# Kernel tuning notes

Hardware: AMD Instinct MI355X
Metric: run time of the kernel (lower is better)

The kernel has to match this reference:

```python
import jax, jax.numpy as jnp
import numpy as np

EMB = 256
HEADS = 8

def setup_inputs() -> dict:
    key = jax.random.key(0)
    k1, k2, k3, k4, k5 = jax.random.split(key, 5)
    b, t = 8, 1024
    scale = 1.0 / np.sqrt(EMB)
    x = jax.random.normal(k1, (b, t, EMB), dtype=jnp.float32)
    # nn.Linear weights stored as [out, in]; we store [in, out] for x @ W
    Wk = jax.random.normal(k2, (EMB, EMB * HEADS), dtype=jnp.float32) * scale
    Wq = jax.random.normal(k3, (EMB, EMB * HEADS), dtype=jnp.float32) * scale
    Wv = jax.random.normal(k4, (EMB, EMB * HEADS), dtype=jnp.float32) * scale
    Wu = jax.random.normal(k5, (EMB * HEADS, EMB), dtype=jnp.float32) * scale
    return {"x": x, "Wq": Wq, "Wk": Wk, "Wv": Wv, "Wu": Wu}

def reference(x, Wq, Wk, Wv, Wu):
    b, t, e = x.shape
    h, d = HEADS, EMB  # per-head dim equals emb_in in this module
    q = (x @ Wq).reshape(b, t, h, d)
    k = (x @ Wk).reshape(b, t, h, d)
    v = (x @ Wv).reshape(b, t, h, d)
    inv4 = d ** (-0.25)
    q = q * inv4
    k = k * inv4
    # scores: [b, h, t, t]
    dot = jnp.einsum('bthd,bshd->bhts', q, k)
    attn = jax.nn.softmax(dot, axis=-1)
    out = jnp.einsum('bhts,bshd->bthd', attn, v).reshape(b, t, h * d)
    return out @ Wu
```

## Files before the change

kernel.cpp:

```cpp
#include <hip/hip_runtime.h>
#include <stdint.h>

typedef unsigned short u16;
typedef __bf16 bf16x8 __attribute__((ext_vector_type(8)));
typedef float f32x4 __attribute__((ext_vector_type(4)));
typedef u16 u16x8 __attribute__((ext_vector_type(8)));

#define MFMA16(a, b, c) __builtin_amdgcn_mfma_f32_16x16x32_bf16((a), (b), (c), 0, 0, 0)

__device__ __forceinline__ u16 f2bf(float f) {
  union { float f; uint32_t u; } v; v.f = f;
  uint32_t u = v.u;
  return (u16)((u + 0x7FFFu + ((u >> 16) & 1u)) >> 16);
}

__device__ __forceinline__ uint32_t pk2(float a, float b) {
  union { __bf16 h[2]; uint32_t u; } v;
  v.h[0] = (__bf16)a; v.h[1] = (__bf16)b;
  return v.u;
}

__device__ __forceinline__ void gload_lds16(const u16* g, u16* l) {
  __builtin_amdgcn_global_load_lds((const __attribute__((address_space(1))) void*)g,
                                   (__attribute__((address_space(3))) void*)l, 16, 0, 0);
}

__global__ __launch_bounds__(256) void prep(const float* __restrict__ x,
                                            const float* __restrict__ Wq,
                                            const float* __restrict__ Wk,
                                            const float* __restrict__ Wv,
                                            const float* __restrict__ Wu,
                                            u16* __restrict__ xb,
                                            u16* __restrict__ WtQ,
                                            u16* __restrict__ WtK,
                                            u16* __restrict__ WtV,
                                            u16* __restrict__ Wut) {
  const int bid = blockIdx.x;
  if (bid < 2048) {
    int i = bid * 256 + threadIdx.x;
    float4 v = ((const float4*)x)[i];
    ushort4 o;
    o.x = f2bf(v.x); o.y = f2bf(v.y); o.z = f2bf(v.z); o.w = f2bf(v.w);
    ((ushort4*)xb)[i] = o;
    return;
  }
  __shared__ float t32[32][33];
  const float* in;
  u16* out;
  int R, C, idx;
  float scale;
  if (bid < 2560)      { idx = bid - 2048; in = Wq; out = WtQ; R = 256;  C = 2048; scale = 0.25f; }
  else if (bid < 3072) { idx = bid - 2560; in = Wk; out = WtK; R = 256;  C = 2048; scale = 0.25f; }
  else if (bid < 3584) { idx = bid - 3072; in = Wv; out = WtV; R = 256;  C = 2048; scale = 1.0f; }
  else                 { idx = bid - 3584; in = Wu; out = Wut; R = 2048; C = 256;  scale = 1.0f; }
  int bx, by;
  if (bid < 3584) { bx = idx & 63; by = idx >> 6; }
  else            { bx = idx & 7;  by = idx >> 3; }
  const int c0 = bx * 32, r0 = by * 32;
  const int tx = threadIdx.x & 31, ty = threadIdx.x >> 5;
  #pragma unroll
  for (int i = 0; i < 32; i += 8)
    t32[ty + i][tx] = in[(size_t)(r0 + ty + i) * C + c0 + tx] * scale;
  __syncthreads();
  #pragma unroll
  for (int i = 0; i < 32; i += 8)
    out[(size_t)(c0 + ty + i) * R + r0 + tx] = f2bf(t32[tx][ty + i]);
}

__global__ __launch_bounds__(256, 2) void gemm_qkv(const u16* __restrict__ A,
                                                   const u16* __restrict__ Bt,
                                                   u16* __restrict__ Qm,
                                                   u16* __restrict__ Km,
                                                   u16* __restrict__ Vtm) {
  __shared__ __attribute__((aligned(16))) u16 As[128 * 32];
  __shared__ __attribute__((aligned(16))) u16 Bs[128 * 32];
  const int tid = threadIdx.x;
  const int lane = tid & 63;
  const int w = tid >> 6;
  const int wr = w >> 1, wc = w & 1;
  const int row0 = blockIdx.y * 128, col0 = blockIdx.x * 128;
  const int rr = lane & 15, kg = lane >> 4;

  f32x4 acc[4][4];
  const f32x4 fz = {0.f, 0.f, 0.f, 0.f};
  #pragma unroll
  for (int m = 0; m < 4; ++m)
    #pragma unroll
    for (int n = 0; n < 4; ++n) acc[m][n] = fz;

  for (int k0 = 0; k0 < 256; k0 += 32) {
    #pragma unroll
    for (int c = 0; c < 2; ++c) {
      int Lb = c * 256 + w * 64;
      int L = Lb + lane;
      int r = L >> 2, cc = L & 3;
      gload_lds16(&A[(size_t)(row0 + r) * 256 + k0 + cc * 8], &As[Lb << 3]);
      gload_lds16(&Bt[(size_t)(col0 + r) * 256 + k0 + cc * 8], &Bs[Lb << 3]);
    }
    __syncthreads();
    bf16x8 af[4], bfr[4];
    #pragma unroll
    for (int m = 0; m < 4; ++m)
      af[m] = *(const bf16x8*)&As[(wr * 64 + m * 16 + rr) * 32 + kg * 8];
    #pragma unroll
    for (int n = 0; n < 4; ++n)
      bfr[n] = *(const bf16x8*)&Bs[(wc * 64 + n * 16 + rr) * 32 + kg * 8];
    #pragma unroll
    for (int m = 0; m < 4; ++m)
      #pragma unroll
      for (int n = 0; n < 4; ++n)
        acc[m][n] = MFMA16(af[m], bfr[n], acc[m][n]);
    __syncthreads();
  }

  #pragma unroll
  for (int m = 0; m < 4; ++m)
    #pragma unroll
    for (int n = 0; n < 4; ++n) {
      int r = row0 + wr * 64 + m * 16 + kg * 4;
      int c = col0 + wc * 64 + n * 16 + rr;
      if (c < 2048) {
        #pragma unroll
        for (int j = 0; j < 4; ++j)
          Qm[(size_t)(r + j) * 2048 + c] = f2bf(acc[m][n][j]);
      } else if (c < 4096) {
        int c2 = c - 2048;
        #pragma unroll
        for (int j = 0; j < 4; ++j)
          Km[(size_t)(r + j) * 2048 + c2] = f2bf(acc[m][n][j]);
      } else {
        int c2 = c - 4096;
        int bb = r >> 10, tt = r & 1023;
        int hh = c2 >> 8, dd = c2 & 255;
        union { u16 h4[4]; uint2 u2; } o4;
        #pragma unroll
        for (int j = 0; j < 4; ++j) o4.h4[j] = f2bf(acc[m][n][j]);
        *(uint2*)&Vtm[(size_t)(bb * 8 + hh) * 262144 + (size_t)dd * 1024 + tt] = o4.u2;
      }
    }
}

template<int FOUT>
__global__ __launch_bounds__(256, 2) void gemm_bt64(const u16* __restrict__ A,
                                                    const u16* __restrict__ Bt,
                                                    void* __restrict__ Cout,
                                                    int M, int N, int K,
                                                    int lda, int ldb, int ldc) {
  __shared__ __attribute__((aligned(16))) u16 As[64 * 32];
  __shared__ __attribute__((aligned(16))) u16 Bs[128 * 32];
  const int tid = threadIdx.x;
  const int lane = tid & 63;
  const int w = tid >> 6;
  const int row0 = blockIdx.y * 64, col0 = blockIdx.x * 128;
  const int rr = lane & 15, kg = lane >> 4;

  f32x4 acc[4][2];
  const f32x4 fz = {0.f, 0.f, 0.f, 0.f};
  #pragma unroll
  for (int m = 0; m < 4; ++m)
    #pragma unroll
    for (int n = 0; n < 2; ++n) acc[m][n] = fz;

  for (int k0 = 0; k0 < K; k0 += 32) {
    {
      int Lb = w * 64;
      int L = Lb + lane;
      int r = L >> 2, cc = L & 3;
      gload_lds16(&A[(size_t)(row0 + r) * lda + k0 + cc * 8], &As[Lb << 3]);
    }
    #pragma unroll
    for (int c = 0; c < 2; ++c) {
      int Lb = c * 256 + w * 64;
      int L = Lb + lane;
      int r = L >> 2, cc = L & 3;
      gload_lds16(&Bt[(size_t)(col0 + r) * ldb + k0 + cc * 8], &Bs[Lb << 3]);
    }
    __syncthreads();
    bf16x8 af[4], bfr[2];
    #pragma unroll
    for (int m = 0; m < 4; ++m)
      af[m] = *(const bf16x8*)&As[(m * 16 + rr) * 32 + kg * 8];
    #pragma unroll
    for (int n = 0; n < 2; ++n)
      bfr[n] = *(const bf16x8*)&Bs[(w * 32 + n * 16 + rr) * 32 + kg * 8];
    #pragma unroll
    for (int m = 0; m < 4; ++m)
      #pragma unroll
      for (int n = 0; n < 2; ++n)
        acc[m][n] = MFMA16(af[m], bfr[n], acc[m][n]);
    __syncthreads();
  }

  #pragma unroll
  for (int m = 0; m < 4; ++m)
    #pragma unroll
    for (int n = 0; n < 2; ++n) {
      int r = row0 + m * 16 + kg * 4;
      int c = col0 + w * 32 + n * 16 + rr;
      #pragma unroll
      for (int j = 0; j < 4; ++j) {
        if (FOUT == 0)
          ((u16*)Cout)[(size_t)(r + j) * ldc + c] = f2bf(acc[m][n][j]);
        else
          ((float*)Cout)[(size_t)(r + j) * ldc + c] = acc[m][n][j];
      }
    }
}

__global__ __launch_bounds__(512) void attn_kernel(const u16* __restrict__ Q,
                                                   const u16* __restrict__ Kg,
                                                   const u16* __restrict__ Vt,
                                                   u16* __restrict__ O) {
  __shared__ __attribute__((aligned(16))) u16 smem[65536];
  u16* Ks = smem;
  u16* Vs = smem + 32768;
  const int tid = threadIdx.x;
  const int lane = tid & 63;
  const int w = tid >> 6;
  const int rr = lane & 15, kg = lane >> 4;
  const int bid = blockIdx.x;
  const int swz = (bid & 7) * 64 + (bid >> 3);
  const int bh = swz >> 3;
  const int b = bh >> 3, h = bh & 7;
  const int q0 = (swz & 7) * 128;
  const u16* Qb = Q + (size_t)b * 1024 * 2048 + (size_t)h * 256;
  const u16* Kb = Kg + (size_t)b * 1024 * 2048 + (size_t)h * 256;
  const u16* Vb = Vt + (size_t)bh * 262144;
  u16* Ob = O + (size_t)b * 1024 * 2048 + (size_t)h * 256;
  const int qrow = q0 + w * 16 + rr;
  const float M0 = 12.0f;

  auto stage_kv = [&](int sb, int s0i) {
    u16* Kd = Ks + sb * 16384;
    u16* Vd = Vs + sb * 16384;
    #pragma unroll
    for (int c = 0; c < 4; ++c) {
      int Lb = (c * 8 + w) * 64;
      int L = Lb + lane;
      int r = L >> 5, cc = L & 31;
      gload_lds16(&Kb[(size_t)(s0i + r) * 2048 + ((cc ^ (r & 7)) << 3)], &Kd[Lb << 3]);
      int rv = L >> 3, cv = L & 7;
      gload_lds16(&Vb[(size_t)rv * 1024 + s0i + ((cv ^ (rv & 7)) << 3)], &Vd[Lb << 3]);
    }
  };

  stage_kv(0, 0);

  bf16x8 qf[8];
  {
    const u16* qp = Qb + (size_t)qrow * 2048;
    #pragma unroll
    for (int kk = 0; kk < 8; ++kk) qf[kk] = *(const bf16x8*)&qp[kk * 32 + kg * 8];
  }

  const f32x4 fz = {0.f, 0.f, 0.f, 0.f};
  f32x4 oacc[16];
  #pragma unroll
  for (int dt = 0; dt < 16; ++dt) oacc[dt] = fz;
  float lrow = 0.f;

  __syncthreads();

  int buf = 0;
  for (int t = 0; t < 16; ++t) {
    if (t < 15) stage_kv(buf ^ 1, (t + 1) * 64);

    const u16* Kd = Ks + buf * 16384;
    f32x4 sacc[4];
    #pragma unroll
    for (int n4 = 0; n4 < 4; ++n4) sacc[n4] = fz;
    __builtin_amdgcn_s_setprio(1);
    #pragma unroll
    for (int kk = 0; kk < 8; ++kk) {
      #pragma unroll
      for (int n4 = 0; n4 < 4; ++n4) {
        int row = n4 * 16 + rr;
        int ck = kk * 4 + kg;
        bf16x8 kf = *(const bf16x8*)&Kd[row * 256 + ((ck ^ (row & 7)) << 3)];
        sacc[n4] = MFMA16(kf, qf[kk], sacc[n4]);
      }
    }
    __builtin_amdgcn_s_setprio(0);

    float sum = 0.f;
    uint32_t L0, H0, L1, H1, L2, H2, L3, H3;
    {
      float e0, e1, e2, e3;
      e0 = __expf(sacc[0][0] - M0); e1 = __expf(sacc[0][1] - M0);
      e2 = __expf(sacc[0][2] - M0); e3 = __expf(sacc[0][3] - M0);
      sum += (e0 + e1) + (e2 + e3); L0 = pk2(e0, e1); H0 = pk2(e2, e3);
      e0 = __expf(sacc[1][0] - M0); e1 = __expf(sacc[1][1] - M0);
      e2 = __expf(sacc[1][2] - M0); e3 = __expf(sacc[1][3] - M0);
      sum += (e0 + e1) + (e2 + e3); L1 = pk2(e0, e1); H1 = pk2(e2, e3);
      e0 = __expf(sacc[2][0] - M0); e1 = __expf(sacc[2][1] - M0);
      e2 = __expf(sacc[2][2] - M0); e3 = __expf(sacc[2][3] - M0);
      sum += (e0 + e1) + (e2 + e3); L2 = pk2(e0, e1); H2 = pk2(e2, e3);
      e0 = __expf(sacc[3][0] - M0); e1 = __expf(sacc[3][1] - M0);
      e2 = __expf(sacc[3][2] - M0); e3 = __expf(sacc[3][3] - M0);
      sum += (e0 + e1) + (e2 + e3); L3 = pk2(e0, e1); H3 = pk2(e2, e3);
    }
    sum += __shfl_xor(sum, 16, 64);
    sum += __shfl_xor(sum, 32, 64);
    lrow += sum;

    const u16* Vd = Vs + buf * 16384;
    const int g = kg;
    #pragma unroll
    for (int t2 = 0; t2 < 2; ++t2) {
      uint32_t La = t2 ? L2 : L0, Ha = t2 ? H2 : H0;
      uint32_t Lb2 = t2 ? L3 : L1, Hb = t2 ? H3 : H1;
      uint32_t La1 = __shfl_xor(La, 16, 64), La2 = __shfl_xor(La, 32, 64);
      uint32_t La3 = __shfl_xor(La1, 32, 64);
      uint32_t Ha1 = __shfl_xor(Ha, 16, 64), Ha2 = __shfl_xor(Ha, 32, 64);
      uint32_t Ha3 = __shfl_xor(Ha1, 32, 64);
      uint32_t Lb1 = __shfl_xor(Lb2, 16, 64), Lb2s = __shfl_xor(Lb2, 32, 64);
      uint32_t Lb3 = __shfl_xor(Lb1, 32, 64);
      uint32_t Hb1 = __shfl_xor(Hb, 16, 64), Hb2 = __shfl_xor(Hb, 32, 64);
      uint32_t Hb3 = __shfl_xor(Hb1, 32, 64);
      uint32_t a2S  = (g == 0) ? La  : (g == 1) ? La3 : (g == 2) ? La2 : La1;
      uint32_t a2S1 = (g == 0) ? La1 : (g == 1) ? La2 : (g == 2) ? La3 : La;
      uint32_t ah2S  = (g == 0) ? Ha  : (g == 1) ? Ha3 : (g == 2) ? Ha2 : Ha1;
      uint32_t ah2S1 = (g == 0) ? Ha1 : (g == 1) ? Ha2 : (g == 2) ? Ha3 : Ha;
      uint32_t b2S  = (g == 0) ? Lb2 : (g == 1) ? Lb3 : (g == 2) ? Lb2s : Lb1;
      uint32_t b2S1 = (g == 0) ? Lb1 : (g == 1) ? Lb2s : (g == 2) ? Lb3 : Lb2;
      uint32_t bh2S  = (g == 0) ? Hb  : (g == 1) ? Hb3 : (g == 2) ? Hb2 : Hb1;
      uint32_t bh2S1 = (g == 0) ? Hb1 : (g == 1) ? Hb2 : (g == 2) ? Hb3 : Hb;
      const int Qn = g >> 1;
      union { uint32_t u[4]; bf16x8 v; } pf;
      pf.u[0] = Qn ? b2S  : a2S;
      pf.u[1] = Qn ? bh2S : ah2S;
      pf.u[2] = Qn ? b2S1 : a2S1;
      pf.u[3] = Qn ? bh2S1 : ah2S1;
      __builtin_amdgcn_s_setprio(1);
      #pragma unroll
      for (int dt = 0; dt < 16; ++dt) {
        int rv = dt * 16 + rr;
        int cv = t2 * 4 + kg;
        bf16x8 vf = *(const bf16x8*)&Vd[rv * 64 + ((cv ^ (rv & 7)) << 3)];
        oacc[dt] = MFMA16(vf, pf.v, oacc[dt]);
      }
      __builtin_amdgcn_s_setprio(0);
    }

    __syncthreads();
    buf ^= 1;
  }

  float inv = 1.0f / lrow;
  #pragma unroll
  for (int dt = 0; dt < 16; ++dt) {
    union { u16 h4[4]; uint2 u2; } o4;
    #pragma unroll
    for (int i = 0; i < 4; ++i) o4.h4[i] = f2bf(oacc[dt][i] * inv);
    *(uint2*)&Ob[(size_t)qrow * 2048 + dt * 16 + kg * 4] = o4.u2;
  }
}

extern "C" void kernel_launch(void* const* d_in, const int* in_sizes, int n_in,
                              void* d_out, int out_size, void* d_ws, size_t ws_size,
                              hipStream_t stream) {
  const float* x  = (const float*)d_in[0];
  const float* Wq = (const float*)d_in[1];
  const float* Wk = (const float*)d_in[2];
  const float* Wv = (const float*)d_in[3];
  const float* Wu = (const float*)d_in[4];

  u16* xb  = (u16*)d_ws;
  u16* WtQ = xb  + 8192 * 256;
  u16* WtK = WtQ + 2048 * 256;
  u16* WtV = WtK + 2048 * 256;
  u16* Wut = WtV + 2048 * 256;
  u16* Qm  = Wut + 2048 * 256;
  u16* Km  = Qm  + (size_t)8192 * 2048;
  u16* Vtm = Km  + (size_t)8192 * 2048;
  u16* Om  = Vtm + (size_t)8192 * 2048;

  prep<<<4096, 256, 0, stream>>>(x, Wq, Wk, Wv, Wu, xb, WtQ, WtK, WtV, Wut);

  gemm_qkv<<<dim3(48, 64), 256, 0, stream>>>(xb, WtQ, Qm, Km, Vtm);

  attn_kernel<<<512, 512, 0, stream>>>(Qm, Km, Vtm, Om);

  gemm_bt64<1><<<dim3(2, 128), 256, 0, stream>>>(Om, Wut, d_out, 8192, 256, 2048, 2048, 2048, 256);
}
```

Baseline: 192.9 us.

## Double-buffer LDS tiles in QKV and output GEMMs to overlap loads

Both GEMM kernels now use two LDS buffers per operand: the next K-slice is issued via global_load_lds into the alternate buffer while MFMAs run on the current one, with a single barrier per step. This aims to hide global-to-LDS latency that previously stalled behind a barrier each iteration. It doubles LDS use per block, which may affect occupancy, and relies on the barrier placement to keep reads and writes on opposite buffers correctly ordered.

```diff
diff --git a/kernel.cpp b/kernel.cpp
--- a/kernel.cpp
+++ b/kernel.cpp
@@ -72,8 +72,8 @@
                                                    u16* __restrict__ Qm,
                                                    u16* __restrict__ Km,
                                                    u16* __restrict__ Vtm) {
-  __shared__ __attribute__((aligned(16))) u16 As[128 * 32];
-  __shared__ __attribute__((aligned(16))) u16 Bs[128 * 32];
+  __shared__ __attribute__((aligned(16))) u16 As[2 * 128 * 32];
+  __shared__ __attribute__((aligned(16))) u16 Bs[2 * 128 * 32];
   const int tid = threadIdx.x;
   const int lane = tid & 63;
   const int w = tid >> 6;
@@ -81,36 +81,48 @@
   const int row0 = blockIdx.y * 128, col0 = blockIdx.x * 128;
   const int rr = lane & 15, kg = lane >> 4;
 
-  f32x4 acc[4][4];
-  const f32x4 fz = {0.f, 0.f, 0.f, 0.f};
-  #pragma unroll
-  for (int m = 0; m < 4; ++m)
-    #pragma unroll
-    for (int n = 0; n < 4; ++n) acc[m][n] = fz;
-
-  for (int k0 = 0; k0 < 256; k0 += 32) {
+  auto stage = [&](int sb, int k0) {
+    u16* Ad = As + sb * 4096;
+    u16* Bd = Bs + sb * 4096;
     #pragma unroll
     for (int c = 0; c < 2; ++c) {
       int Lb = c * 256 + w * 64;
       int L = Lb + lane;
       int r = L >> 2, cc = L & 3;
-      gload_lds16(&A[(size_t)(row0 + r) * 256 + k0 + cc * 8], &As[Lb << 3]);
-      gload_lds16(&Bt[(size_t)(col0 + r) * 256 + k0 + cc * 8], &Bs[Lb << 3]);
-    }
-    __syncthreads();
+      gload_lds16(&A[(size_t)(row0 + r) * 256 + k0 + cc * 8], &Ad[Lb << 3]);
+      gload_lds16(&Bt[(size_t)(col0 + r) * 256 + k0 + cc * 8], &Bd[Lb << 3]);
+    }
+  };
+
+  f32x4 acc[4][4];
+  const f32x4 fz = {0.f, 0.f, 0.f, 0.f};
+  #pragma unroll
+  for (int m = 0; m < 4; ++m)
+    #pragma unroll
+    for (int n = 0; n < 4; ++n) acc[m][n] = fz;
+
+  stage(0, 0);
+  __syncthreads();
+
+  int buf = 0;
+  for (int s = 0; s < 8; ++s) {
+    if (s < 7) stage(buf ^ 1, (s + 1) * 32);
+    const u16* Ar = As + buf * 4096;
+    const u16* Br = Bs + buf * 4096;
     bf16x8 af[4], bfr[4];
     #pragma unroll
     for (int m = 0; m < 4; ++m)
-      af[m] = *(const bf16x8*)&As[(wr * 64 + m * 16 + rr) * 32 + kg * 8];
+      af[m] = *(const bf16x8*)&Ar[(wr * 64 + m * 16 + rr) * 32 + kg * 8];
     #pragma unroll
     for (int n = 0; n < 4; ++n)
-      bfr[n] = *(const bf16x8*)&Bs[(wc * 64 + n * 16 + rr) * 32 + kg * 8];
+      bfr[n] = *(const bf16x8*)&Br[(wc * 64 + n * 16 + rr) * 32 + kg * 8];
     #pragma unroll
     for (int m = 0; m < 4; ++m)
       #pragma unroll
       for (int n = 0; n < 4; ++n)
         acc[m][n] = MFMA16(af[m], bfr[n], acc[m][n]);
     __syncthreads();
+    buf ^= 1;
   }
 
   #pragma unroll
@@ -146,49 +158,62 @@
                                                     void* __restrict__ Cout,
                                                     int M, int N, int K,
                                                     int lda, int ldb, int ldc) {
-  __shared__ __attribute__((aligned(16))) u16 As[64 * 32];
-  __shared__ __attribute__((aligned(16))) u16 Bs[128 * 32];
+  __shared__ __attribute__((aligned(16))) u16 As[2 * 64 * 32];
+  __shared__ __attribute__((aligned(16))) u16 Bs[2 * 128 * 32];
   const int tid = threadIdx.x;
   const int lane = tid & 63;
   const int w = tid >> 6;
   const int row0 = blockIdx.y * 64, col0 = blockIdx.x * 128;
   const int rr = lane & 15, kg = lane >> 4;
 
-  f32x4 acc[4][2];
-  const f32x4 fz = {0.f, 0.f, 0.f, 0.f};
-  #pragma unroll
-  for (int m = 0; m < 4; ++m)
-    #pragma unroll
-    for (int n = 0; n < 2; ++n) acc[m][n] = fz;
-
-  for (int k0 = 0; k0 < K; k0 += 32) {
+  auto stage = [&](int sb, int k0) {
+    u16* Ad = As + sb * 2048;
+    u16* Bd = Bs + sb * 4096;
     {
       int Lb = w * 64;
       int L = Lb + lane;
       int r = L >> 2, cc = L & 3;
-      gload_lds16(&A[(size_t)(row0 + r) * lda + k0 + cc * 8], &As[Lb << 3]);
+      gload_lds16(&A[(size_t)(row0 + r) * lda + k0 + cc * 8], &Ad[Lb << 3]);
     }
     #pragma unroll
     for (int c = 0; c < 2; ++c) {
       int Lb = c * 256 + w * 64;
       int L = Lb + lane;
       int r = L >> 2, cc = L & 3;
-      gload_lds16(&Bt[(size_t)(col0 + r) * ldb + k0 + cc * 8], &Bs[Lb << 3]);
-    }
-    __syncthreads();
+      gload_lds16(&Bt[(size_t)(col0 + r) * ldb + k0 + cc * 8], &Bd[Lb << 3]);
+    }
+  };
+
+  f32x4 acc[4][2];
+  const f32x4 fz = {0.f, 0.f, 0.f, 0.f};
+  #pragma unroll
+  for (int m = 0; m < 4; ++m)
+    #pragma unroll
+    for (int n = 0; n < 2; ++n) acc[m][n] = fz;
+
+  stage(0, 0);
+  __syncthreads();
+
+  const int nsteps = K / 32;
+  int buf = 0;
+  for (int s = 0; s < nsteps; ++s) {
+    if (s < nsteps - 1) stage(buf ^ 1, (s + 1) * 32);
+    const u16* Ar = As + buf * 2048;
+    const u16* Br = Bs + buf * 4096;
     bf16x8 af[4], bfr[2];
     #pragma unroll
     for (int m = 0; m < 4; ++m)
-      af[m] = *(const bf16x8*)&As[(m * 16 + rr) * 32 + kg * 8];
+      af[m] = *(const bf16x8*)&Ar[(m * 16 + rr) * 32 + kg * 8];
     #pragma unroll
     for (int n = 0; n < 2; ++n)
-      bfr[n] = *(const bf16x8*)&Bs[(w * 32 + n * 16 + rr) * 32 + kg * 8];
+      bfr[n] = *(const bf16x8*)&Br[(w * 32 + n * 16 + rr) * 32 + kg * 8];
     #pragma unroll
     for (int m = 0; m < 4; ++m)
       #pragma unroll
       for (int n = 0; n < 2; ++n)
         acc[m][n] = MFMA16(af[m], bfr[n], acc[m][n]);
     __syncthreads();
+    buf ^= 1;
   }
 
   #pragma unroll
```

Result: no change. 191.4 us, median of 2 (-0.8%).
